# Kernel optimization log

Measured on AMD Instinct MI355X. Metric: run time of the kernel, lower is better.

Reference implementation:

```python
import jax, jax.numpy as jnp
import numpy as np

B, INPUT_SIZE, HIDDEN, OUT, K = 16, 8192, 8, 34, 5
N = B * INPUT_SIZE            # 131072 nodes
E = N * 32                    # 4194304 edges


def setup_inputs() -> dict:
    key = jax.random.key(0)
    ks = jax.random.split(key, 8)
    x = jax.random.normal(ks[0], (N, 1), dtype=jnp.float32)
    edge_index = jax.random.randint(ks[1], (2, E), 0, N, dtype=jnp.int64)
    edge_attr = jax.random.normal(ks[2], (E,), dtype=jnp.float32)  # unused by forward, kept for signature fidelity
    batch = jnp.repeat(jnp.arange(B, dtype=jnp.int64), INPUT_SIZE)
    W1 = jax.random.normal(ks[3], (K, 1, HIDDEN), dtype=jnp.float32) * 0.3
    b1 = jnp.zeros((HIDDEN,), jnp.float32)
    W2 = jax.random.normal(ks[4], (K, HIDDEN, HIDDEN), dtype=jnp.float32) * 0.2
    b2 = jnp.zeros((HIDDEN,), jnp.float32)
    lin1_w = jax.random.normal(ks[5], (HIDDEN * INPUT_SIZE, 1000), dtype=jnp.float32) * 0.004
    lin1_b = jnp.zeros((1000,), jnp.float32)
    lin2_w = jax.random.normal(ks[6], (1000, OUT), dtype=jnp.float32) * 0.03
    lin2_b = jnp.zeros((OUT,), jnp.float32)
    return dict(x=x, edge_index=edge_index, edge_attr=edge_attr, batch=batch,
                W1=W1, b1=b1, W2=W2, b2=b2,
                lin1_w=lin1_w, lin1_b=lin1_b, lin2_w=lin2_w, lin2_b=lin2_b)


def _cheb_setup(edge_index, n, dtype):
    # PyG ChebConv with sym norm, lambda_max=2: Lhat = -D^{-1/2} A D^{-1/2},
    # diag 0 for deg>0 nodes, -1 for isolated nodes. Self loops removed.
    row, col = edge_index[0], edge_index[1]
    w = (row != col).astype(dtype)                      # remove self loops via zero weight
    deg = jax.ops.segment_sum(w, row, num_segments=n)
    dinv = jnp.where(deg > 0, jax.lax.rsqrt(jnp.maximum(deg, 1.0)), 0.0)
    norm = -dinv[row] * w * dinv[col]                   # [E]
    diag = jnp.where(deg > 0, 0.0, -1.0)[:, None]       # [N,1]
    return row, col, norm, diag


def _cheb_conv(x, W, b, row, col, norm, diag, n):
    # out = sum_k T_k(Lhat) x @ W[k] + b, Chebyshev recurrence over K slices
    def lhat(t):  # sparse matvec: scatter-add of weighted source features
        return jax.ops.segment_sum(norm[:, None] * t[row], col, num_segments=n) + diag * t
    Tx0 = x
    out = Tx0 @ W[0]
    Tx1 = lhat(Tx0)
    out = out + Tx1 @ W[1]
    for k in range(2, W.shape[0]):
        Tx2 = 2.0 * lhat(Tx1) - Tx0
        out = out + Tx2 @ W[k]
        Tx0, Tx1 = Tx1, Tx2
    return out + b


def reference(x, edge_index, edge_attr, batch, W1, b1, W2, b2, lin1_w, lin1_b, lin2_w, lin2_b):
    n = x.shape[0]
    row, col, norm, diag = _cheb_setup(edge_index, n, x.dtype)
    h = jax.nn.relu(_cheb_conv(x, W1, b1, row, col, norm, diag, n))
    h = jax.nn.relu(_cheb_conv(h, W2, b2, row, col, norm, diag, n))
    hidden = W2.shape[2]
    input_size = lin1_w.shape[0] // hidden
    bsz = n // input_size                                # == max(batch)+1
    h = h.reshape(bsz, input_size * hidden)
    h = jax.nn.relu(h @ lin1_w + lin1_b)
    return jnp.squeeze(h @ lin2_w + lin2_b)
```

## Files before the change

### kernel.cpp

```cpp
#include <hip/hip_runtime.h>

#define NN 131072
#define NE 4194304
#define HID 8
#define BSZ 16
#define MDIM 1000
#define ODIM 34
#define FC 128
#define NCHUNK 512
#define NB 1024
#define EPB (NE / NB)
#define NBUK 1024
#define CNOD 128
#define NBUKR 512
#define SCAP 6144

typedef float f4v __attribute__((ext_vector_type(4)));
typedef float f2v __attribute__((ext_vector_type(2)));
typedef _Float16 h8v __attribute__((ext_vector_type(8)));

__global__ __launch_bounds__(512) void bin_count(const int* __restrict__ ei,
                                                 int* __restrict__ colhist,
                                                 int* __restrict__ rowhist) {
    __shared__ int ch[NBUK];
    __shared__ int rh[NBUKR];
    int b = blockIdx.x, t = threadIdx.x;
    for (int i = t; i < NBUK; i += 512) ch[i] = 0;
    for (int i = t; i < NBUKR; i += 512) rh[i] = 0;
    __syncthreads();
    int base = b * EPB;
    for (int k = t; k < EPB; k += 512) {
        int e = base + k;
        int r = __builtin_nontemporal_load(&ei[e]);
        int c = __builtin_nontemporal_load(&ei[NE + e]);
        if (r != c) { atomicAdd(&ch[c >> 7], 1); atomicAdd(&rh[r >> 8], 1); }
    }
    __syncthreads();
    for (int i = t; i < NBUK; i += 512) colhist[b * NBUK + i] = ch[i];
    for (int i = t; i < NBUKR; i += 512) rowhist[b * NBUKR + i] = rh[i];
}

__global__ __launch_bounds__(NB) void bin_scan(int* __restrict__ hist,
                                               int* __restrict__ tot, int nbuckets) {
    __shared__ int s[NB];
    int i = blockIdx.x, t = threadIdx.x;
    int v = hist[(size_t)t * nbuckets + i];
    s[t] = v; __syncthreads();
    for (int off = 1; off < NB; off <<= 1) {
        int x = (t >= off) ? s[t - off] : 0;
        __syncthreads(); s[t] += x; __syncthreads();
    }
    hist[(size_t)t * nbuckets + i] = s[t] - v;
    if (t == NB - 1) tot[i] = s[t];
}

template <int M>
__global__ __launch_bounds__(256) void base_scan(const int* __restrict__ tot,
                                                 int* __restrict__ basev) {
    __shared__ int s[256];
    int t = threadIdx.x;
    int v[M]; int ps = 0;
    #pragma unroll
    for (int q = 0; q < M; ++q) { v[q] = tot[t * M + q]; ps += v[q]; }
    s[t] = ps; __syncthreads();
    for (int off = 1; off < 256; off <<= 1) {
        int x = (t >= off) ? s[t - off] : 0;
        __syncthreads(); s[t] += x; __syncthreads();
    }
    int run = s[t] - ps;
    #pragma unroll
    for (int q = 0; q < M; ++q) { basev[t * M + q] = run; run += v[q]; }
}

__global__ __launch_bounds__(512) void bin_fill(const int* __restrict__ ei,
                                                const int* __restrict__ colhist,
                                                const int* __restrict__ rowhist,
                                                const int* __restrict__ colbase,
                                                const int* __restrict__ rowbase,
                                                unsigned int* __restrict__ colbinned,
                                                unsigned char* __restrict__ rowbinned) {
    __shared__ int cc[NBUK];
    __shared__ int rc[NBUKR];
    int b = blockIdx.x, t = threadIdx.x;
    for (int i = t; i < NBUK; i += 512) cc[i] = colbase[i] + colhist[b * NBUK + i];
    for (int i = t; i < NBUKR; i += 512) rc[i] = rowbase[i] + rowhist[b * NBUKR + i];
    __syncthreads();
    int base = b * EPB;
    for (int k = t; k < EPB; k += 512) {
        int e = base + k;
        int r = __builtin_nontemporal_load(&ei[e]);
        int c = __builtin_nontemporal_load(&ei[NE + e]);
        if (r != c) {
            int p = atomicAdd(&cc[c >> 7], 1);
            colbinned[p] = ((unsigned)r << 7) | (unsigned)(c & 127);
            int q = atomicAdd(&rc[r >> 8], 1);
            rowbinned[q] = (unsigned char)(r & 255);
        }
    }
}

__global__ __launch_bounds__(256) void bucket_sort2(unsigned int* __restrict__ colbinned,
                                                    const int* __restrict__ colbase,
                                                    const int* __restrict__ coltot,
                                                    int* __restrict__ o,
                                                    int* __restrict__ sflag) {
    __shared__ unsigned int recs[SCAP];
    __shared__ int cnt[CNOD], scn[CNOD], cur[CNOD];
    int b = blockIdx.x, t = threadIdx.x;
    int s0 = colbase[b], n = coltot[b];
    if (n > SCAP) {
        if (t == 0) sflag[b] = 1;
        for (int i = t; i < CNOD; i += 256) o[b * CNOD + i] = s0;
        if (b == NBUK - 1 && t == 0) o[NN] = s0 + n;
        return;
    }
    if (t == 0) sflag[b] = 0;
    for (int i = t; i < CNOD; i += 256) cnt[i] = 0;
    __syncthreads();
    for (int i = t; i < n; i += 256) {
        unsigned int rec = colbinned[s0 + i];
        recs[i] = rec;
        atomicAdd(&cnt[rec & 127], 1);
    }
    __syncthreads();
    if (t < CNOD) scn[t] = cnt[t];
    __syncthreads();
    for (int off = 1; off < CNOD; off <<= 1) {
        int v = 0;
        if (t < CNOD && t >= off) v = scn[t - off];
        __syncthreads();
        if (t < CNOD) scn[t] += v;
        __syncthreads();
    }
    if (t < CNOD) {
        int ex = scn[t] - cnt[t];
        cur[t] = ex;
        o[b * CNOD + t] = s0 + ex;
    }
    __syncthreads();
    if (b == NBUK - 1 && t == 0) o[NN] = s0 + n;
    for (int i = t; i < n; i += 256) {
        unsigned int rec = recs[i];
        int p = atomicAdd(&cur[rec & 127], 1);
        colbinned[s0 + p] = rec;
    }
}

__global__ __launch_bounds__(256) void deg_finish(const unsigned char* __restrict__ rowbinned,
                                                  const int* __restrict__ rowbase,
                                                  const int* __restrict__ rowtot,
                                                  const float* __restrict__ x,
                                                  float* __restrict__ dinv,
                                                  float* __restrict__ rinv,
                                                  float* __restrict__ sx) {
    __shared__ int cnt[256];
    int b = blockIdx.x, t = threadIdx.x;
    cnt[t] = 0; __syncthreads();
    int s0 = rowbase[b], n = rowtot[b];
    for (int i = t; i < n; i += 256) atomicAdd(&cnt[rowbinned[s0 + i]], 1);
    __syncthreads();
    int d = cnt[t];
    int node = b * 256 + t;
    float dn = (d > 0) ? rsqrtf((float)d) : 0.f;
    dinv[node] = dn;
    rinv[node] = (d > 0) ? sqrtf((float)d) : 1.f;
    sx[node] = ((d > 0) ? dn : 1.f) * x[node];
}

template <int MODE>
__global__ __launch_bounds__(512) void cheb1_s(const unsigned int* __restrict__ colbinned,
                                               const int* __restrict__ colbase,
                                               const int* __restrict__ coltot,
                                               const int* __restrict__ o,
                                               const int* __restrict__ sflag,
                                               const float* __restrict__ dinv,
                                               const float* __restrict__ w_in,
                                               const float* __restrict__ wp2,
                                               float* __restrict__ w_out) {
    __shared__ float part[CNOD][4];
    __shared__ float accA[CNOD];
    int b = blockIdx.x, t = threadIdx.x;
    if (sflag[b]) {
        if (t < CNOD) accA[t] = 0.f;
        __syncthreads();
        int s0 = colbase[b], n = coltot[b];
        for (int i = t; i < n; i += 512) {
            unsigned int rec = colbinned[s0 + i];
            atomicAdd(&accA[rec & 127], w_in[rec >> 7]);
        }
        __syncthreads();
        if (t < CNOD) { part[t][0] = accA[t]; part[t][1] = 0.f; part[t][2] = 0.f; part[t][3] = 0.f; }
    } else {
        int nl = t >> 2, q = t & 3;
        int node = b * CNOD + nl;
        int os = o[node], oe = o[node + 1];
        float a = 0.f;
        for (int i = os + q; i < oe; i += 4) {
            unsigned int rec = __builtin_nontemporal_load(&colbinned[i]);
            a += w_in[rec >> 7];
        }
        part[nl][q] = a;
    }
    __syncthreads();
    if (t < CNOD) {
        float a = part[t][0] + part[t][1] + part[t][2] + part[t][3];
        int node = b * CNOD + t;
        float dn = dinv[node];
        float lh = (dn > 0.f) ? -dn * a : -w_in[node];
        float s = (dn > 0.f) ? dn : 1.f;
        w_out[node] = (MODE == 0) ? s * lh : s * (2.f * lh) - wp2[node];
    }
}

__global__ __launch_bounds__(256) void h1_kernel(const float* __restrict__ x,
        const float* __restrict__ wt1, const float* __restrict__ wt2,
        const float* __restrict__ wt3, const float* __restrict__ wt4,
        const float* __restrict__ dinv, const float* __restrict__ rinv,
        const float* __restrict__ W1, const float* __restrict__ b1,
        const float* __restrict__ W20, const float* __restrict__ b2,
        float* __restrict__ sh1, _Float16* __restrict__ s1t,
        float* __restrict__ accg) {
    int n = blockIdx.x * 256 + threadIdx.x;
    float rn = rinv[n], dn = dinv[n];
    float s = (dn > 0.f) ? dn : 1.f;
    float T0 = x[n], T1 = wt1[n] * rn, T2 = wt2[n] * rn, T3 = wt3[n] * rn, T4 = wt4[n] * rn;
    float h[HID];
    #pragma unroll
    for (int j = 0; j < HID; ++j) {
        float v = b1[j] + T0 * W1[j] + T1 * W1[8 + j] + T2 * W1[16 + j]
                + T3 * W1[24 + j] + T4 * W1[32 + j];
        h[j] = fmaxf(v, 0.f);
    }
    f4v sv0, sv1, av0, av1;
    h8v hv;
    #pragma unroll
    for (int j = 0; j < 4; ++j) { sv0[j] = s * h[j]; sv1[j] = s * h[4 + j]; }
    #pragma unroll
    for (int j = 0; j < 8; ++j) hv[j] = (_Float16)(s * h[j]);
    #pragma unroll
    for (int o2 = 0; o2 < HID; ++o2) {
        float v = b2[o2];
        #pragma unroll
        for (int j = 0; j < HID; ++j) v = fmaf(h[j], W20[j * 8 + o2], v);
        if (o2 < 4) av0[o2] = v; else av1[o2 - 4] = v;
    }
    *(f4v*)&sh1[n * 8] = sv0;  *(f4v*)&sh1[n * 8 + 4] = sv1;
    *(h8v*)&s1t[n * 8] = hv;
    *(f4v*)&accg[n * 8] = av0; *(f4v*)&accg[n * 8 + 4] = av1;
}

template <int MODE>
__global__ __launch_bounds__(512) void cheb8_e(const unsigned int* __restrict__ colbinned,
        const int* __restrict__ colbase, const int* __restrict__ coltot,
        const int* __restrict__ o, const int* __restrict__ sflag,
        const float* __restrict__ dinv, const float* __restrict__ rinv,
        const _Float16* __restrict__ w16_in, const float* __restrict__ w_in,
        const float* __restrict__ wp2,
        float* __restrict__ w_out, _Float16* __restrict__ w16_out,
        const float* __restrict__ Wk, float* __restrict__ accg) {
    __shared__ float pl[CNOD][4][9];
    __shared__ float vb[CNOD][HID];
    __shared__ float wk[64];
    __shared__ float accA[CNOD * 9];
    int b = blockIdx.x, t = threadIdx.x;
    if (t < 64) wk[t] = Wk[t];
    int nl = t >> 2, l = t & 3;
    int node = b * CNOD + nl;
    float a[8];
    #pragma unroll
    for (int j = 0; j < 8; ++j) a[j] = 0.f;
    if (!sflag[b]) {
        int os = o[node], oe = o[node + 1];
        for (int i = os + l; i < oe; i += 4) {
            unsigned int rec = __builtin_nontemporal_load(&colbinned[i]);
            h8v hv = *(const h8v*)&w16_in[(rec >> 7) * 8];
            #pragma unroll
            for (int j = 0; j < 8; ++j) a[j] += (float)hv[j];
        }
    } else {
        for (int i2 = t; i2 < CNOD * 9; i2 += 512) accA[i2] = 0.f;
        __syncthreads();
        int s0 = colbase[b], n = coltot[b];
        for (int i = t; i < n; i += 512) {
            unsigned int rec = colbinned[s0 + i];
            int r = rec >> 7, cl = rec & 127;
            h8v hv = *(const h8v*)&w16_in[r * 8];
            float* ap = &accA[cl * 9];
            #pragma unroll
            for (int j = 0; j < 8; ++j) atomicAdd(ap + j, (float)hv[j]);
        }
        __syncthreads();
        if (l == 0) {
            #pragma unroll
            for (int j = 0; j < 8; ++j) a[j] = accA[nl * 9 + j];
        }
    }
    #pragma unroll
    for (int j = 0; j < 8; ++j) pl[nl][l][j] = a[j];
    __syncthreads();
    #pragma unroll
    for (int k2 = 0; k2 < 2; ++k2) {
        int idx = k2 * 512 + t;
        int n2 = idx >> 3, jj = idx & 7;
        int nd = b * CNOD + n2;
        float asum = pl[n2][0][jj] + pl[n2][1][jj] + pl[n2][2][jj] + pl[n2][3][jj];
        float dn = dinv[nd];
        float lh = (dn > 0.f) ? -dn * asum : -w_in[nd * 8 + jj];
        float T;
        if (MODE == 0) {
            T = lh;
            float w = (dn > 0.f) ? dn * lh : lh;
            w_out[nd * 8 + jj] = w;
            w16_out[nd * 8 + jj] = (_Float16)w;
        } else if (MODE == 1) {
            float sc = (dn > 0.f) ? dn : 1.f;
            float w = sc * (2.f * lh) - wp2[nd * 8 + jj];
            w_out[nd * 8 + jj] = w;
            w16_out[nd * 8 + jj] = (_Float16)w;
            T = w * rinv[nd];
        } else {
            T = 2.f * lh - wp2[nd * 8 + jj] * rinv[nd];
        }
        vb[n2][jj] = T;
    }
    __syncthreads();
    #pragma unroll
    for (int k2 = 0; k2 < 2; ++k2) {
        int idx = k2 * 512 + t;
        int n2 = idx >> 3, jj = idx & 7;
        int nd = b * CNOD + n2;
        float sum = 0.f;
        #pragma unroll
        for (int q = 0; q < HID; ++q) sum = fmaf(vb[n2][q], wk[q * 8 + jj], sum);
        float r2 = accg[nd * 8 + jj] + sum;
        accg[nd * 8 + jj] = (MODE == 2) ? fmaxf(r2, 0.f) : r2;
    }
}

__global__ __launch_bounds__(256) void lin1_kernel(const float* __restrict__ h2,
                                                   const float* __restrict__ w,
                                                   float* __restrict__ part) {
    int chunk = blockIdx.x, t = threadIdx.x;
    int fbase = chunk * FC;
    __shared__ __align__(16) float a[FC * 20];
    for (int i = t; i < BSZ * FC; i += 256) {
        int bb = i >> 7, f = i & (FC - 1);
        a[f * 20 + bb] = h2[(size_t)bb * 65536 + fbase + f];
    }
    __syncthreads();
    f4v acc[16];
    #pragma unroll
    for (int bb = 0; bb < 16; ++bb) acc[bb] = (f4v)(0.f);
    int m = t * 4;
    if (m < MDIM) {
        for (int f = 0; f < FC; ++f) {
            f4v wv = __builtin_nontemporal_load((const f4v*)&w[(size_t)(fbase + f) * MDIM + m]);
            const f4v* ar = (const f4v*)&a[f * 20];
            f4v a0 = ar[0], a1 = ar[1], a2 = ar[2], a3 = ar[3];
            acc[0] += a0.x * wv;  acc[1] += a0.y * wv;  acc[2] += a0.z * wv;  acc[3] += a0.w * wv;
            acc[4] += a1.x * wv;  acc[5] += a1.y * wv;  acc[6] += a1.z * wv;  acc[7] += a1.w * wv;
            acc[8] += a2.x * wv;  acc[9] += a2.y * wv;  acc[10] += a2.z * wv; acc[11] += a2.w * wv;
            acc[12] += a3.x * wv; acc[13] += a3.y * wv; acc[14] += a3.z * wv; acc[15] += a3.w * wv;
        }
    }
    #pragma unroll
    for (int bb = 0; bb < 16; ++bb) {
        __builtin_nontemporal_store(acc[bb], (f4v*)&part[((size_t)chunk * 16 + bb) * 1024 + m]);
    }
}

__global__ __launch_bounds__(256) void hidden1(const float* __restrict__ part,
                                               float* __restrict__ part2) {
    int g = blockIdx.x >> 6;
    int off = (blockIdx.x & 63) * 256 + threadIdx.x;
    float s = 0.f;
    const float* p = part + (size_t)g * 64 * 16384 + off;
    for (int c = 0; c < 64; ++c) s += __builtin_nontemporal_load(&p[c * 16384]);
    part2[g * 16384 + off] = s;
}

__global__ __launch_bounds__(256) void hidden2(const float* __restrict__ part2,
                                               const float* __restrict__ lb,
                                               float* __restrict__ hid) {
    int off = blockIdx.x * 256 + threadIdx.x;
    int b = off >> 10, m = off & 1023;
    if (m >= MDIM) return;
    float s = lb[m];
    for (int g = 0; g < 8; ++g) s += part2[g * 16384 + off];
    hid[b * MDIM + m] = fmaxf(s, 0.f);
}

__global__ void out_kernel(const float* __restrict__ hid, const float* __restrict__ w2,
                           const float* __restrict__ b2, float* __restrict__ out) {
    int i = blockIdx.x * blockDim.x + threadIdx.x;
    if (i >= BSZ * ODIM) return;
    int b = i / ODIM, o = i % ODIM;
    float s = b2[o];
    for (int m = 0; m < MDIM; ++m) s = fmaf(hid[b * MDIM + m], w2[m * ODIM + o], s);
    out[i] = s;
}

extern "C" void kernel_launch(void* const* d_in, const int* in_sizes, int n_in,
                              void* d_out, int out_size, void* d_ws, size_t ws_size,
                              hipStream_t stream) {
    const float* x      = (const float*)d_in[0];
    const int*   ei     = (const int*)d_in[1];
    const float* W1     = (const float*)d_in[4];
    const float* b1     = (const float*)d_in[5];
    const float* W2     = (const float*)d_in[6];
    const float* b2     = (const float*)d_in[7];
    const float* lin1w  = (const float*)d_in[8];
    const float* lin1b  = (const float*)d_in[9];
    const float* lin2w  = (const float*)d_in[10];
    const float* lin2b  = (const float*)d_in[11];
    float* out = (float*)d_out;

    unsigned int* colbinned = (unsigned int*)d_ws;
    _Float16* s1t = (_Float16*)(colbinned + NE);
    _Float16* s2t = s1t + 8 * (size_t)NN;
    unsigned char* rowbinned = (unsigned char*)(s2t + 8 * (size_t)NN);
    float* wA   = (float*)(rowbinned + NE);
    float* wB   = wA + 8 * (size_t)NN;
    float* sh1  = wB + 8 * (size_t)NN;
    float* wt1  = sh1 + 8 * (size_t)NN;
    float* wt2  = wt1 + NN;
    float* wt3  = wt2 + NN;
    float* wt4  = wt3 + NN;
    float* sx   = wt4 + NN;
    float* dinv = sx + NN;
    float* rinv = dinv + NN;
    int* colhist = (int*)(rinv + NN);
    int* rowhist = colhist + (size_t)NB * NBUK;
    int* coltot  = rowhist + (size_t)NB * NBUKR;
    int* colbase = coltot + NBUK;
    int* rowtot  = colbase + NBUK;
    int* rowbase = rowtot + NBUKR;
    int* o       = rowbase + NBUKR;
    int* sflag   = o + NN + 1;
    float* accg  = (float*)(sflag + NBUK);
    float* hid   = accg + 8 * (size_t)NN;
    float* part2 = hid + BSZ * 1024;
    float* part  = part2 + 8 * 16384;

    bin_count<<<NB, 512, 0, stream>>>(ei, colhist, rowhist);
    bin_scan<<<NBUK, NB, 0, stream>>>(colhist, coltot, NBUK);
    bin_scan<<<NBUKR, NB, 0, stream>>>(rowhist, rowtot, NBUKR);
    base_scan<4><<<1, 256, 0, stream>>>(coltot, colbase);
    base_scan<2><<<1, 256, 0, stream>>>(rowtot, rowbase);
    bin_fill<<<NB, 512, 0, stream>>>(ei, colhist, rowhist, colbase, rowbase, colbinned, rowbinned);
    bucket_sort2<<<NBUK, 256, 0, stream>>>(colbinned, colbase, coltot, o, sflag);
    deg_finish<<<NBUKR, 256, 0, stream>>>(rowbinned, rowbase, rowtot, x, dinv, rinv, sx);

    cheb1_s<0><<<NBUK, 512, 0, stream>>>(colbinned, colbase, coltot, o, sflag, dinv, sx, nullptr, wt1);
    cheb1_s<1><<<NBUK, 512, 0, stream>>>(colbinned, colbase, coltot, o, sflag, dinv, wt1, sx, wt2);
    cheb1_s<1><<<NBUK, 512, 0, stream>>>(colbinned, colbase, coltot, o, sflag, dinv, wt2, wt1, wt3);
    cheb1_s<1><<<NBUK, 512, 0, stream>>>(colbinned, colbase, coltot, o, sflag, dinv, wt3, wt2, wt4);
    h1_kernel<<<NN / 256, 256, 0, stream>>>(x, wt1, wt2, wt3, wt4, dinv, rinv,
                                            W1, b1, W2, b2, sh1, s1t, accg);

    cheb8_e<0><<<NBUK, 512, 0, stream>>>(colbinned, colbase, coltot, o, sflag, dinv, rinv,
                                         s1t, sh1, nullptr, wA, s2t, W2 + 64, accg);
    cheb8_e<1><<<NBUK, 512, 0, stream>>>(colbinned, colbase, coltot, o, sflag, dinv, rinv,
                                         s2t, wA, sh1, wB, s1t, W2 + 128, accg);
    cheb8_e<1><<<NBUK, 512, 0, stream>>>(colbinned, colbase, coltot, o, sflag, dinv, rinv,
                                         s1t, wB, wA, wA, s2t, W2 + 192, accg);
    cheb8_e<2><<<NBUK, 512, 0, stream>>>(colbinned, colbase, coltot, o, sflag, dinv, rinv,
                                         s2t, wA, wB, nullptr, nullptr, W2 + 256, accg);

    lin1_kernel<<<NCHUNK, 256, 0, stream>>>(accg, lin1w, part);
    hidden1<<<512, 256, 0, stream>>>(part, part2);
    hidden2<<<64, 256, 0, stream>>>(part2, lin1b, hid);
    out_kernel<<<3, 256, 0, stream>>>(hid, lin2w, lin2b, out);
}
```

Baseline: 624.1 us.

## Fuse Chebyshev passes into one persistent cooperative kernel with grid sync

Replaces the nine separate Chebyshev launches (four scalar passes, the h1 layer, four 8-wide passes) with one cooperative kernel of 512 blocks. Each block covers two buckets, and grid.sync separates the recurrence steps. The aim is to remove kernel launch gaps and tail effects between the dependent passes. In exchange, the grid runs with fewer blocks and less latency hiding per pass, grid-wide barriers add their own cost, and the old launches remain as a fallback if the cooperative launch fails.

Measured after the change: 1.874 ms. 200% more time.

```diff
diff --git a/kernel.cpp b/kernel.cpp
--- a/kernel.cpp
+++ b/kernel.cpp
@@ -1,4 +1,7 @@
 #include <hip/hip_runtime.h>
+#include <hip/hip_cooperative_groups.h>
+
+namespace cg = cooperative_groups;
 
 #define NN 131072
 #define NE 4194304
@@ -14,9 +17,9 @@
 #define CNOD 128
 #define NBUKR 512
 #define SCAP 6144
+#define MGRID 512
 
 typedef float f4v __attribute__((ext_vector_type(4)));
-typedef float f2v __attribute__((ext_vector_type(2)));
 typedef _Float16 h8v __attribute__((ext_vector_type(8)));
 
 __global__ __launch_bounds__(512) void bin_count(const int* __restrict__ ei,
@@ -165,6 +168,193 @@
     dinv[node] = dn;
     rinv[node] = (d > 0) ? sqrtf((float)d) : 1.f;
     sx[node] = ((d > 0) ? dn : 1.f) * x[node];
+}
+
+struct MegaP {
+    const unsigned int* colbinned;
+    const int* colbase; const int* coltot; const int* o; const int* sflag;
+    const float* dinv; const float* rinv;
+    const float* x; const float* sx;
+    float* wt1; float* wt2; float* wt3; float* wt4;
+    const float* W1; const float* b1; const float* W2; const float* b2;
+    float* sh1; _Float16* s1t; _Float16* s2t;
+    float* wA; float* wB; float* accg;
+};
+
+__global__ __launch_bounds__(512, 4) void cheb_mega(MegaP p) {
+    cg::grid_group grid = cg::this_grid();
+    __shared__ float vb[CNOD][HID];
+    __shared__ float wkL[64];
+    __shared__ float accF[CNOD * 9];
+    int blk = blockIdx.x, t = threadIdx.x;
+    int nl = t >> 2, l = t & 3;
+
+    const float* w1in[4]  = { p.sx, p.wt1, p.wt2, p.wt3 };
+    const float* w1p2[4]  = { nullptr, p.sx, p.wt1, p.wt2 };
+    float*       w1out[4] = { p.wt1, p.wt2, p.wt3, p.wt4 };
+    #pragma unroll
+    for (int ps = 0; ps < 4; ++ps) {
+        const float* win = w1in[ps];
+        const float* wp2 = w1p2[ps];
+        float* wout = w1out[ps];
+        for (int bk = 0; bk < 2; ++bk) {
+            int b = blk * 2 + bk;
+            int nb = b * CNOD;
+            int node = nb + nl;
+            float a = 0.f;
+            if (!p.sflag[b]) {
+                int i0 = p.o[node], i1 = p.o[node + 1];
+                for (int i = i0 + l; i < i1; i += 4)
+                    a += win[__builtin_nontemporal_load(&p.colbinned[i]) >> 7];
+            } else {
+                for (int i = t; i < CNOD; i += 512) accF[i] = 0.f;
+                __syncthreads();
+                int s0 = p.colbase[b], n = p.coltot[b];
+                for (int i = t; i < n; i += 512) {
+                    unsigned int rec = p.colbinned[s0 + i];
+                    atomicAdd(&accF[rec & 127], win[rec >> 7]);
+                }
+                __syncthreads();
+                if (l == 0) a = accF[nl];
+                __syncthreads();
+            }
+            a += __shfl_xor(a, 1);
+            a += __shfl_xor(a, 2);
+            if (l == 0) {
+                float dn = p.dinv[node];
+                float lh = (dn > 0.f) ? -dn * a : -win[node];
+                float s = (dn > 0.f) ? dn : 1.f;
+                wout[node] = (ps == 0) ? s * lh : s * (2.f * lh) - wp2[node];
+            }
+        }
+        __threadfence();
+        grid.sync();
+    }
+
+    if (t < 256) {
+        int n = blk * 256 + t;
+        float rn = p.rinv[n], dn = p.dinv[n];
+        float s = (dn > 0.f) ? dn : 1.f;
+        float T0 = p.x[n], T1 = p.wt1[n] * rn, T2 = p.wt2[n] * rn,
+              T3 = p.wt3[n] * rn, T4 = p.wt4[n] * rn;
+        float h[HID];
+        #pragma unroll
+        for (int j = 0; j < HID; ++j) {
+            float v = p.b1[j] + T0 * p.W1[j] + T1 * p.W1[8 + j] + T2 * p.W1[16 + j]
+                    + T3 * p.W1[24 + j] + T4 * p.W1[32 + j];
+            h[j] = fmaxf(v, 0.f);
+        }
+        f4v sv0, sv1, av0, av1;
+        h8v hv;
+        #pragma unroll
+        for (int j = 0; j < 4; ++j) { sv0[j] = s * h[j]; sv1[j] = s * h[4 + j]; }
+        #pragma unroll
+        for (int j = 0; j < 8; ++j) hv[j] = (_Float16)(s * h[j]);
+        #pragma unroll
+        for (int o2 = 0; o2 < HID; ++o2) {
+            float v = p.b2[o2];
+            #pragma unroll
+            for (int j = 0; j < HID; ++j) v = fmaf(h[j], p.W2[j * 8 + o2], v);
+            if (o2 < 4) av0[o2] = v; else av1[o2 - 4] = v;
+        }
+        *(f4v*)&p.sh1[n * 8] = sv0;  *(f4v*)&p.sh1[n * 8 + 4] = sv1;
+        *(h8v*)&p.s1t[n * 8] = hv;
+        *(f4v*)&p.accg[n * 8] = av0; *(f4v*)&p.accg[n * 8 + 4] = av1;
+    }
+    __threadfence();
+    grid.sync();
+
+    const _Float16* w2in16[4]  = { p.s1t, p.s2t, p.s1t, p.s2t };
+    const float*    w2in[4]    = { p.sh1, p.wA, p.wB, p.wA };
+    const float*    w2p2[4]    = { nullptr, p.sh1, p.wA, p.wB };
+    float*          w2out[4]   = { p.wA, p.wB, p.wA, nullptr };
+    _Float16*       w2out16[4] = { p.s2t, p.s1t, p.s2t, nullptr };
+    #pragma unroll
+    for (int ps = 0; ps < 4; ++ps) {
+        const _Float16* win16 = w2in16[ps];
+        const float* wfp = w2in[ps];
+        const float* wp2 = w2p2[ps];
+        float* wo = w2out[ps];
+        _Float16* wo16 = w2out16[ps];
+        if (t < 64) wkL[t] = p.W2[64 * (ps + 1) + t];
+        for (int bk = 0; bk < 2; ++bk) {
+            int b = blk * 2 + bk;
+            int nb = b * CNOD;
+            int node = nb + nl;
+            float a[8];
+            #pragma unroll
+            for (int j = 0; j < 8; ++j) a[j] = 0.f;
+            if (!p.sflag[b]) {
+                int i0 = p.o[node], i1 = p.o[node + 1];
+                for (int i = i0 + l; i < i1; i += 4) {
+                    unsigned int rec = __builtin_nontemporal_load(&p.colbinned[i]);
+                    h8v v = *(const h8v*)&win16[(rec >> 7) * 8];
+                    #pragma unroll
+                    for (int j = 0; j < 8; ++j) a[j] += (float)v[j];
+                }
+            } else {
+                for (int i = t; i < CNOD * 9; i += 512) accF[i] = 0.f;
+                __syncthreads();
+                int s0 = p.colbase[b], n = p.coltot[b];
+                for (int i = t; i < n; i += 512) {
+                    unsigned int rec = p.colbinned[s0 + i];
+                    h8v v = *(const h8v*)&win16[(rec >> 7) * 8];
+                    float* ap = &accF[(rec & 127) * 9];
+                    #pragma unroll
+                    for (int j = 0; j < 8; ++j) atomicAdd(ap + j, (float)v[j]);
+                }
+                __syncthreads();
+                if (l == 0) {
+                    #pragma unroll
+                    for (int j = 0; j < 8; ++j) a[j] = accF[nl * 9 + j];
+                }
+                __syncthreads();
+            }
+            #pragma unroll
+            for (int j = 0; j < 8; ++j) {
+                a[j] += __shfl_xor(a[j], 1);
+                a[j] += __shfl_xor(a[j], 2);
+            }
+            if (l == 0) {
+                float dn = p.dinv[node];
+                float rn = p.rinv[node];
+                #pragma unroll
+                for (int j = 0; j < 8; ++j) {
+                    float lh = (dn > 0.f) ? -dn * a[j] : -wfp[node * 8 + j];
+                    float T;
+                    if (ps == 0) {
+                        T = lh;
+                        float w = (dn > 0.f) ? dn * lh : lh;
+                        wo[node * 8 + j] = w;
+                        wo16[node * 8 + j] = (_Float16)w;
+                    } else if (ps < 3) {
+                        float sc = (dn > 0.f) ? dn : 1.f;
+                        float w = sc * (2.f * lh) - wp2[node * 8 + j];
+                        wo[node * 8 + j] = w;
+                        wo16[node * 8 + j] = (_Float16)w;
+                        T = w * rn;
+                    } else {
+                        T = 2.f * lh - wp2[node * 8 + j] * rn;
+                    }
+                    vb[nl][j] = T;
+                }
+            }
+            __syncthreads();
+            #pragma unroll
+            for (int k2 = 0; k2 < 2; ++k2) {
+                int idx = k2 * 512 + t;
+                int n2 = idx >> 3, jj = idx & 7;
+                int nd = nb + n2;
+                float sum = 0.f;
+                #pragma unroll
+                for (int q = 0; q < HID; ++q) sum = fmaf(vb[n2][q], wkL[q * 8 + jj], sum);
+                float r2 = p.accg[nd * 8 + jj] + sum;
+                p.accg[nd * 8 + jj] = (ps == 3) ? fmaxf(r2, 0.f) : r2;
+            }
+            __syncthreads();
+        }
+        if (ps < 3) { __threadfence(); grid.sync(); }
+    }
 }
 
 template <int MODE>
@@ -195,10 +385,8 @@
         int node = b * CNOD + nl;
         int os = o[node], oe = o[node + 1];
         float a = 0.f;
-        for (int i = os + q; i < oe; i += 4) {
-            unsigned int rec = __builtin_nontemporal_load(&colbinned[i]);
-            a += w_in[rec >> 7];
-        }
+        for (int i = os + q; i < oe; i += 4)
+            a += w_in[__builtin_nontemporal_load(&colbinned[i]) >> 7];
         part[nl][q] = a;
     }
     __syncthreads();
@@ -283,9 +471,8 @@
         int s0 = colbase[b], n = coltot[b];
         for (int i = t; i < n; i += 512) {
             unsigned int rec = colbinned[s0 + i];
-            int r = rec >> 7, cl = rec & 127;
-            h8v hv = *(const h8v*)&w16_in[r * 8];
-            float* ap = &accA[cl * 9];
+            h8v hv = *(const h8v*)&w16_in[(rec >> 7) * 8];
+            float* ap = &accA[(rec & 127) * 9];
             #pragma unroll
             for (int j = 0; j < 8; ++j) atomicAdd(ap + j, (float)hv[j]);
         }
@@ -451,21 +638,33 @@
     bucket_sort2<<<NBUK, 256, 0, stream>>>(colbinned, colbase, coltot, o, sflag);
     deg_finish<<<NBUKR, 256, 0, stream>>>(rowbinned, rowbase, rowtot, x, dinv, rinv, sx);
 
-    cheb1_s<0><<<NBUK, 512, 0, stream>>>(colbinned, colbase, coltot, o, sflag, dinv, sx, nullptr, wt1);
-    cheb1_s<1><<<NBUK, 512, 0, stream>>>(colbinned, colbase, coltot, o, sflag, dinv, wt1, sx, wt2);
-    cheb1_s<1><<<NBUK, 512, 0, stream>>>(colbinned, colbase, coltot, o, sflag, dinv, wt2, wt1, wt3);
-    cheb1_s<1><<<NBUK, 512, 0, stream>>>(colbinned, colbase, coltot, o, sflag, dinv, wt3, wt2, wt4);
-    h1_kernel<<<NN / 256, 256, 0, stream>>>(x, wt1, wt2, wt3, wt4, dinv, rinv,
-                                            W1, b1, W2, b2, sh1, s1t, accg);
-
-    cheb8_e<0><<<NBUK, 512, 0, stream>>>(colbinned, colbase, coltot, o, sflag, dinv, rinv,
-                                         s1t, sh1, nullptr, wA, s2t, W2 + 64, accg);
-    cheb8_e<1><<<NBUK, 512, 0, stream>>>(colbinned, colbase, coltot, o, sflag, dinv, rinv,
-                                         s2t, wA, sh1, wB, s1t, W2 + 128, accg);
-    cheb8_e<1><<<NBUK, 512, 0, stream>>>(colbinned, colbase, coltot, o, sflag, dinv, rinv,
-                                         s1t, wB, wA, wA, s2t, W2 + 192, accg);
-    cheb8_e<2><<<NBUK, 512, 0, stream>>>(colbinned, colbase, coltot, o, sflag, dinv, rinv,
-                                         s2t, wA, wB, nullptr, nullptr, W2 + 256, accg);
+    MegaP mp;
+    mp.colbinned = colbinned; mp.colbase = colbase; mp.coltot = coltot;
+    mp.o = o; mp.sflag = sflag;
+    mp.dinv = dinv; mp.rinv = rinv; mp.x = x; mp.sx = sx;
+    mp.wt1 = wt1; mp.wt2 = wt2; mp.wt3 = wt3; mp.wt4 = wt4;
+    mp.W1 = W1; mp.b1 = b1; mp.W2 = W2; mp.b2 = b2;
+    mp.sh1 = sh1; mp.s1t = s1t; mp.s2t = s2t;
+    mp.wA = wA; mp.wB = wB; mp.accg = accg;
+    void* kargs[] = { &mp };
+    hipError_t cerr = hipLaunchCooperativeKernel((const void*)cheb_mega,
+                                                 dim3(MGRID), dim3(512), kargs, 0, stream);
+    if (cerr != hipSuccess) {
+        cheb1_s<0><<<NBUK, 512, 0, stream>>>(colbinned, colbase, coltot, o, sflag, dinv, sx, nullptr, wt1);
+        cheb1_s<1><<<NBUK, 512, 0, stream>>>(colbinned, colbase, coltot, o, sflag, dinv, wt1, sx, wt2);
+        cheb1_s<1><<<NBUK, 512, 0, stream>>>(colbinned, colbase, coltot, o, sflag, dinv, wt2, wt1, wt3);
+        cheb1_s<1><<<NBUK, 512, 0, stream>>>(colbinned, colbase, coltot, o, sflag, dinv, wt3, wt2, wt4);
+        h1_kernel<<<NN / 256, 256, 0, stream>>>(x, wt1, wt2, wt3, wt4, dinv, rinv,
+                                                W1, b1, W2, b2, sh1, s1t, accg);
+        cheb8_e<0><<<NBUK, 512, 0, stream>>>(colbinned, colbase, coltot, o, sflag, dinv, rinv,
+                                             s1t, sh1, nullptr, wA, s2t, W2 + 64, accg);
+        cheb8_e<1><<<NBUK, 512, 0, stream>>>(colbinned, colbase, coltot, o, sflag, dinv, rinv,
+                                             s2t, wA, sh1, wB, s1t, W2 + 128, accg);
+        cheb8_e<1><<<NBUK, 512, 0, stream>>>(colbinned, colbase, coltot, o, sflag, dinv, rinv,
+                                             s1t, wB, wA, wA, s2t, W2 + 192, accg);
+        cheb8_e<2><<<NBUK, 512, 0, stream>>>(colbinned, colbase, coltot, o, sflag, dinv, rinv,
+                                             s2t, wA, wB, nullptr, nullptr, W2 + 256, accg);
+    }
 
     lin1_kernel<<<NCHUNK, 256, 0, stream>>>(accg, lin1w, part);
     hidden1<<<512, 256, 0, stream>>>(part, part2);
```
